# Optimization experiments

Hardware: AMD Instinct MI355X
Metric: run time of the kernel (lower is better)

The kernel has to match this reference:

```python
import jax, jax.numpy as jnp
import numpy as np

B, L, C = 512, 2048, 32  # batch, seq_len, num_labels


def setup_inputs() -> dict:
    key = jax.random.key(0)
    k1, k2, k3 = jax.random.split(key, 3)
    emissions = jax.random.normal(k1, (B, L, C), dtype=jnp.float32)
    tags = jax.random.randint(k2, (B, L), 0, C, dtype=jnp.int32)
    mask = jnp.ones((B, L), dtype=jnp.int32)
    # learned parameter: transitions (num_labels, num_labels)
    transitions = jax.random.normal(k3, (C, C), dtype=jnp.float32)
    return {"emissions": emissions, "transitions": transitions, "tags": tags, "mask": mask}


def _crf_nll(emissions, transitions, tags, mask):
    Bn, Ln, Cn = emissions.shape
    maskf = mask.astype(emissions.dtype)

    # ---- gold-path score (vectorized over the t loop) ----
    # emit[b,t] = emissions[b,t,tags[b,t]] for t in [0, L-2]
    emit = jnp.take_along_axis(emissions[:, : Ln - 1], tags[:, : Ln - 1, None], axis=2)[..., 0]
    # trans[b,t] = transitions[tags[b,t], tags[b,t+1]]
    trans = transitions[tags[:, : Ln - 1], tags[:, 1:]]
    score = jnp.sum(emit * maskf[:, : Ln - 1] + trans * maskf[:, 1:], axis=1)

    msum = jnp.sum(mask, axis=1)
    last_idx = jnp.clip(msum - 1, 0)  # index of last valid tag
    last_tag = jnp.take_along_axis(tags, last_idx[:, None], axis=1)[:, 0]
    le_t = jnp.clip(msum, 1) - 1
    last_emission = emissions[jnp.arange(Bn), le_t, last_tag]
    score = score + last_emission

    # ---- log-partition via forward algorithm (lax.scan over time) ----
    # Faithful to source: alpha_t[b,n,p] = alpha[b,p] + transitions[n,p] + emit[b,n],
    # reduced over p; the source's mask line is an algebraic no-op (a*m + a*(1-m) = a).
    def step(alpha, emit_t):
        # alpha: (B, C) over prev label p; emit_t: (B, C) over next label n
        alpha_new = jax.nn.logsumexp(alpha[:, None, :] + transitions[None, :, :], axis=2) + emit_t
        return alpha_new, None

    alpha0 = emissions[:, 0]                      # (B, C)
    em_rest = jnp.swapaxes(emissions[:, 1:], 0, 1)  # (L-1, B, C)
    alpha, _ = jax.lax.scan(step, alpha0, em_rest)
    log_Z = jax.nn.logsumexp(alpha, axis=1)       # (B,)

    return jnp.mean(log_Z - score)


def reference(emissions, transitions, tags, mask):
    return _crf_nll(emissions, transitions, tags, mask)
```

## Files before the change

kernel.cpp:

```cpp
#include <hip/hip_runtime.h>
#include <stdint.h>

typedef short bf16x8 __attribute__((ext_vector_type(8)));
typedef float f32x16 __attribute__((ext_vector_type(16)));

#define LOG2E 1.44269504088896340736f

constexpr int Bn = 512;
constexpr int Ln = 2048;
constexpr int Cn = 32;
constexpr int NSEG = 256;
constexpr int SEGLEN = 8;
constexpr int WARM = 8;
constexpr int NGRP = 16;
constexpr int DEPTH = 3;

__device__ __forceinline__ uint32_t pack2_bf16(float lo, float hi) {
    uint32_t a = __float_as_uint(lo) + 0x8000u;
    uint32_t b = __float_as_uint(hi) + 0x8000u;
    return __builtin_amdgcn_perm(b, a, 0x07060302u);
}

__global__ __launch_bounds__(64, 4) void crf_scan(
    const float* __restrict__ emis, const float* __restrict__ trans,
    float* __restrict__ dDelta)
{
    const int lane = threadIdx.x;
    const int h    = lane >> 5;
    const int bl   = lane & 31;
    const int g    = blockIdx.x & (NGRP - 1);
    const int s    = blockIdx.x >> 4;
    const int b    = g * 32 + bl;
    const size_t eb = (size_t)b * Ln * Cn;

    bf16x8 A1, A2;
    {
        float e1[8], e2[8];
        #pragma unroll
        for (int j = 0; j < 8; ++j) {
            int c1 = 4 * h + (j & 3) + 8 * (j >> 2);
            e1[j] = __expf(trans[bl * Cn + c1]);
            e2[j] = __expf(trans[bl * Cn + c1 + 16]);
        }
        union { uint32_t u[4]; bf16x8 v; } ua, ub;
        #pragma unroll
        for (int q = 0; q < 4; ++q) {
            ua.u[q] = pack2_bf16(e1[2*q], e1[2*q+1]);
            ub.u[q] = pack2_bf16(e2[2*q], e2[2*q+1]);
        }
        A1 = ua.v; A2 = ub.v;
    }

    const f32x16 zeroC = {0.f,0.f,0.f,0.f,0.f,0.f,0.f,0.f,0.f,0.f,0.f,0.f,0.f,0.f,0.f,0.f};

    f32x16 Dv;
    bf16x8 B1, B2;
    float adj = 0.f;
    float4 buf[DEPTH][4];

    const int t0 = (s == 0) ? 0 : s * SEGLEN - WARM;
    const int nsteps = (s == 0) ? SEGLEN : (WARM + SEGLEN);

    auto loadEm = [&](int t, float4 (&dst)[4]) {
        const float4* p = (const float4*)(emis + eb + (size_t)t * Cn + 4 * h);
        dst[0] = p[0]; dst[1] = p[2]; dst[2] = p[4]; dst[3] = p[6];
    };

    auto packB = [&]() {
        union { uint32_t u[4]; bf16x8 v; } p1, p2;
        #pragma unroll
        for (int q = 0; q < 4; ++q) {
            p1.u[q] = pack2_bf16(Dv[2*q],     Dv[2*q + 1]);
            p2.u[q] = pack2_bf16(Dv[8 + 2*q], Dv[8 + 2*q + 1]);
        }
        B1 = p1.v; B2 = p2.v;
    };

    auto initStep = [&](const float4 (&bu)[4]) {
        #pragma unroll
        for (int q = 0; q < 4; ++q) {
            Dv[4*q+0] = __expf(bu[q].x);
            Dv[4*q+1] = __expf(bu[q].y);
            Dv[4*q+2] = __expf(bu[q].z);
            Dv[4*q+3] = __expf(bu[q].w);
        }
        packB();
    };

    auto stepMfma = [&](const float4 (&bu)[4], float a) {
        f32x16 acc = __builtin_amdgcn_mfma_f32_32x32x16_bf16(A1, B1, zeroC, 0, 0, 0);
        acc = __builtin_amdgcn_mfma_f32_32x32x16_bf16(A2, B2, acc, 0, 0, 0);
        #pragma unroll
        for (int q = 0; q < 4; ++q) {
            float x0 = exp2f(fmaf(bu[q].x, LOG2E, a));
            float x1 = exp2f(fmaf(bu[q].y, LOG2E, a));
            float x2 = exp2f(fmaf(bu[q].z, LOG2E, a));
            float x3 = exp2f(fmaf(bu[q].w, LOG2E, a));
            Dv[4*q+0] = acc[4*q+0] * x0;
            Dv[4*q+1] = acc[4*q+1] * x1;
            Dv[4*q+2] = acc[4*q+2] * x2;
            Dv[4*q+3] = acc[4*q+3] * x3;
        }
        packB();
    };

    auto sumD = [&]() {
        float t = 0.f;
        #pragma unroll
        for (int r = 0; r < 16; ++r) t += Dv[r];
        t += __shfl_xor(t, 32, 64);
        return t;
    };

    #pragma unroll
    for (int u = 0; u < DEPTH; ++u) loadEm(t0 + u, buf[u]);

    if (s == 0) {
        initStep(buf[0]);
        loadEm(t0 + DEPTH, buf[0]);
        #pragma unroll
        for (int u = 1; u < SEGLEN; ++u) {
            stepMfma(buf[u % DEPTH], 0.f);
            if (u + DEPTH < SEGLEN) loadEm(t0 + DEPTH + u, buf[u % DEPTH]);
        }
    } else {
        initStep(buf[0]);
        loadEm(t0 + DEPTH, buf[0]);
        #pragma unroll
        for (int u = 1; u < WARM; ++u) {
            stepMfma(buf[u % DEPTH], 0.f);
            loadEm(t0 + DEPTH + u, buf[u % DEPTH]);
        }
        float S = sumD();
        adj = -__log2f(S);
        #pragma unroll
        for (int u = WARM; u < WARM + SEGLEN; ++u) {
            stepMfma(buf[u % DEPTH], (u == WARM) ? adj : 0.f);
            if (u + DEPTH < WARM + SEGLEN) loadEm(t0 + DEPTH + u, buf[u % DEPTH]);
        }
    }

    float delta = __logf(sumD());
    if (lane < 32) dDelta[s * Bn + b] = delta;
}

__global__ __launch_bounds__(256) void crf_score(
    const float* __restrict__ emis, const float* __restrict__ trans,
    const int* __restrict__ tags, const int* __restrict__ mask,
    float* __restrict__ dScoreP, int* __restrict__ dMsumP)
{
    __shared__ float Tl[Cn * Cn];
    __shared__ float sred[4];
    __shared__ int   mred[4];
    const int b   = blockIdx.x >> 2;
    const int q   = blockIdx.x & 3;
    const int tid = threadIdx.x;
    for (int i = tid; i < Cn * Cn; i += 256) Tl[i] = trans[i];
    __syncthreads();

    const size_t tB = (size_t)b * Ln;
    const size_t eB = (size_t)b * Ln * Cn;
    float sc = 0.f;
    int   ms = 0;
    #pragma unroll
    for (int k = 0; k < 2; ++k) {
        int t  = q * 512 + k * 256 + tid;
        int tg = tags[tB + t];
        int mk = mask[tB + t];
        ms += mk;
        if (t < Ln - 1) {
            int tg1 = tags[tB + t + 1];
            int mk1 = mask[tB + t + 1];
            sc += (float)mk  * emis[eB + (size_t)t * Cn + tg];
            sc += (float)mk1 * Tl[(tg << 5) + tg1];
        }
    }
    #pragma unroll
    for (int o = 32; o > 0; o >>= 1) {
        sc += __shfl_down(sc, o, 64);
        ms += __shfl_down(ms, o, 64);
    }
    if ((tid & 63) == 0) { sred[tid >> 6] = sc; mred[tid >> 6] = ms; }
    __syncthreads();
    if (tid == 0) {
        float S = 0.f; int M = 0;
        #pragma unroll
        for (int w = 0; w < 4; ++w) { S += sred[w]; M += mred[w]; }
        dScoreP[blockIdx.x] = S;
        dMsumP [blockIdx.x] = M;
    }
}

__global__ void crf_final(const float* __restrict__ dDelta,
                          const float* __restrict__ dScoreP,
                          const int* __restrict__ dMsumP,
                          const int* __restrict__ tags,
                          const float* __restrict__ emis,
                          float* __restrict__ out)
{
    __shared__ float red[8];
    int b = threadIdx.x;
    float lz = 0.f;
    #pragma unroll 8
    for (int s2 = 0; s2 < NSEG; ++s2) lz += dDelta[s2 * Bn + b];
    float sc = 0.f; int ms = 0;
    #pragma unroll
    for (int q = 0; q < 4; ++q) { sc += dScoreP[b * 4 + q]; ms += dMsumP[b * 4 + q]; }
    int last_idx = max(ms - 1, 0);
    int le_t     = max(ms, 1) - 1;
    int lt = tags[(size_t)b * Ln + last_idx];
    float le = emis[((size_t)b * Ln + le_t) * Cn + lt];
    float val = lz - (sc + le);
    #pragma unroll
    for (int o = 32; o > 0; o >>= 1) val += __shfl_down(val, o, 64);
    if ((b & 63) == 0) red[b >> 6] = val;
    __syncthreads();
    if (b == 0) {
        float t = 0.f;
        #pragma unroll
        for (int w = 0; w < 8; ++w) t += red[w];
        out[0] = t * (1.0f / (float)Bn);
    }
}

extern "C" void kernel_launch(void* const* d_in, const int* in_sizes, int n_in,
                              void* d_out, int out_size, void* d_ws, size_t ws_size,
                              hipStream_t stream)
{
    const float* emis  = (const float*)d_in[0];
    const float* trans = (const float*)d_in[1];
    const int*   tags  = (const int*)d_in[2];
    const int*   mask  = (const int*)d_in[3];
    float* wsf = (float*)d_ws;
    float* dDelta  = wsf;
    float* dScoreP = wsf + NSEG * Bn;
    int*   dMsumP  = (int*)(wsf + NSEG * Bn + 2048);
    crf_scan <<<NGRP * NSEG, 64, 0, stream>>>(emis, trans, dDelta);
    crf_score<<<4 * Bn, 256, 0, stream>>>(emis, trans, tags, mask, dScoreP, dMsumP);
    crf_final<<<1, Bn, 0, stream>>>(dDelta, dScoreP, dMsumP, tags, emis, (float*)d_out);
}
```

Baseline: 249.8 us.

## Fuse gold-path scoring into scan kernel and lengthen segments to cut warmup overhead

Removes the separate crf_score kernel. The gold-path score and mask sum are now computed inside crf_scan from emission values already loaded for the forward recurrence, using a cross-half shuffle to select the tag's emission. Segments grow from 8 to 16 steps with 128 segments, so the fixed 8-step warmup is paid over more useful steps, and the prefetch depth rises to 8. The cost is more registers per thread (occupancy hint lowered to 2), extra shuffles and LDS transition lookups inside the recurrence, and a larger per-segment reduction in crf_final.

```diff
diff --git a/kernel.cpp b/kernel.cpp
--- a/kernel.cpp
+++ b/kernel.cpp
@@ -9,11 +9,11 @@
 constexpr int Bn = 512;
 constexpr int Ln = 2048;
 constexpr int Cn = 32;
-constexpr int NSEG = 256;
-constexpr int SEGLEN = 8;
+constexpr int NSEG = 128;
+constexpr int SEGLEN = 16;
 constexpr int WARM = 8;
 constexpr int NGRP = 16;
-constexpr int DEPTH = 3;
+constexpr int DEPTH = 8;
 
 __device__ __forceinline__ uint32_t pack2_bf16(float lo, float hi) {
     uint32_t a = __float_as_uint(lo) + 0x8000u;
@@ -21,10 +21,12 @@
     return __builtin_amdgcn_perm(b, a, 0x07060302u);
 }
 
-__global__ __launch_bounds__(64, 4) void crf_scan(
+__global__ __launch_bounds__(64, 2) void crf_scan(
     const float* __restrict__ emis, const float* __restrict__ trans,
-    float* __restrict__ dDelta)
+    const int* __restrict__ tags, const int* __restrict__ mask,
+    float* __restrict__ dDelta, float* __restrict__ dScore, int* __restrict__ dMsum)
 {
+    __shared__ float Tl[Cn * Cn];
     const int lane = threadIdx.x;
     const int h    = lane >> 5;
     const int bl   = lane & 31;
@@ -32,6 +34,31 @@
     const int s    = blockIdx.x >> 4;
     const int b    = g * 32 + bl;
     const size_t eb = (size_t)b * Ln * Cn;
+    const size_t tB = (size_t)b * Ln;
+
+    for (int i = lane; i < Cn * Cn; i += 64) Tl[i] = trans[i];
+
+    const int rt0 = s * SEGLEN;
+    int tg[16], mk[16];
+    {
+        int4 a0 = *(const int4*)(tags + tB + rt0);
+        int4 a1 = *(const int4*)(tags + tB + rt0 + 4);
+        int4 a2 = *(const int4*)(tags + tB + rt0 + 8);
+        int4 a3 = *(const int4*)(tags + tB + rt0 + 12);
+        int4 c0 = *(const int4*)(mask + tB + rt0);
+        int4 c1 = *(const int4*)(mask + tB + rt0 + 4);
+        int4 c2 = *(const int4*)(mask + tB + rt0 + 8);
+        int4 c3 = *(const int4*)(mask + tB + rt0 + 12);
+        tg[0]=a0.x; tg[1]=a0.y; tg[2]=a0.z; tg[3]=a0.w;
+        tg[4]=a1.x; tg[5]=a1.y; tg[6]=a1.z; tg[7]=a1.w;
+        tg[8]=a2.x; tg[9]=a2.y; tg[10]=a2.z; tg[11]=a2.w;
+        tg[12]=a3.x; tg[13]=a3.y; tg[14]=a3.z; tg[15]=a3.w;
+        mk[0]=c0.x; mk[1]=c0.y; mk[2]=c0.z; mk[3]=c0.w;
+        mk[4]=c1.x; mk[5]=c1.y; mk[6]=c1.z; mk[7]=c1.w;
+        mk[8]=c2.x; mk[9]=c2.y; mk[10]=c2.z; mk[11]=c2.w;
+        mk[12]=c3.x; mk[13]=c3.y; mk[14]=c3.z; mk[15]=c3.w;
+    }
+    int prevTag = (s > 0) ? tags[tB + rt0 - 1] : 0;
 
     bf16x8 A1, A2;
     {
@@ -56,10 +83,11 @@
     f32x16 Dv;
     bf16x8 B1, B2;
     float adj = 0.f;
+    float sc  = 0.f;
+    int   ms  = 0;
     float4 buf[DEPTH][4];
 
-    const int t0 = (s == 0) ? 0 : s * SEGLEN - WARM;
-    const int nsteps = (s == 0) ? SEGLEN : (WARM + SEGLEN);
+    const int t0 = (s == 0) ? 0 : rt0 - WARM;
 
     auto loadEm = [&](int t, float4 (&dst)[4]) {
         const float4* p = (const float4*)(emis + eb + (size_t)t * Cn + 4 * h);
@@ -112,100 +140,93 @@
         return t;
     };
 
+    auto emitSel = [&](const float4 (&bu)[4], int tag) -> float {
+        float4 f01 = (tag & 8)  ? bu[1] : bu[0];
+        float4 f23 = (tag & 8)  ? bu[3] : bu[2];
+        float4 f   = (tag & 16) ? f23 : f01;
+        float  v0  = (tag & 1)  ? f.y : f.x;
+        float  v1  = (tag & 1)  ? f.w : f.z;
+        float  v   = (tag & 2)  ? v1 : v0;
+        float  other = __shfl_xor(v, 32, 64);
+        return (((tag >> 2) & 1) == h) ? v : other;
+    };
+
+    auto scoreStep = [&](const float4 (&bu)[4], int u) {
+        int t  = rt0 + u;
+        int tgv = tg[u], mkv = mk[u];
+        float term = 0.f;
+        if (t > 0)      term += Tl[(prevTag << 5) + tgv];
+        if (t < Ln - 1) term += emitSel(bu, tgv);
+        sc += (float)mkv * term;
+        ms += mkv;
+        prevTag = tgv;
+    };
+
     #pragma unroll
     for (int u = 0; u < DEPTH; ++u) loadEm(t0 + u, buf[u]);
 
     if (s == 0) {
+        scoreStep(buf[0], 0);
         initStep(buf[0]);
-        loadEm(t0 + DEPTH, buf[0]);
-        #pragma unroll
-        for (int u = 1; u < SEGLEN; ++u) {
-            stepMfma(buf[u % DEPTH], 0.f);
-            if (u + DEPTH < SEGLEN) loadEm(t0 + DEPTH + u, buf[u % DEPTH]);
+        loadEm(8, buf[0]);
+        #pragma unroll
+        for (int u = 1; u < 8; ++u) {
+            scoreStep(buf[u], u);
+            stepMfma(buf[u], 0.f);
+            loadEm(8 + u, buf[u]);
+        }
+        #pragma unroll
+        for (int u = 8; u < 16; ++u) {
+            scoreStep(buf[u & 7], u);
+            stepMfma(buf[u & 7], 0.f);
         }
     } else {
         initStep(buf[0]);
-        loadEm(t0 + DEPTH, buf[0]);
+        loadEm(t0 + 8, buf[0]);
         #pragma unroll
         for (int u = 1; u < WARM; ++u) {
-            stepMfma(buf[u % DEPTH], 0.f);
-            loadEm(t0 + DEPTH + u, buf[u % DEPTH]);
+            stepMfma(buf[u], 0.f);
+            loadEm(t0 + 8 + u, buf[u]);
         }
         float S = sumD();
         adj = -__log2f(S);
         #pragma unroll
-        for (int u = WARM; u < WARM + SEGLEN; ++u) {
-            stepMfma(buf[u % DEPTH], (u == WARM) ? adj : 0.f);
-            if (u + DEPTH < WARM + SEGLEN) loadEm(t0 + DEPTH + u, buf[u % DEPTH]);
+        for (int u = 0; u < 8; ++u) {
+            scoreStep(buf[u], u);
+            stepMfma(buf[u], (u == 0) ? adj : 0.f);
+            loadEm(rt0 + 8 + u, buf[u]);
+        }
+        #pragma unroll
+        for (int u = 8; u < 16; ++u) {
+            scoreStep(buf[u & 7], u);
+            stepMfma(buf[u & 7], 0.f);
         }
     }
 
     float delta = __logf(sumD());
-    if (lane < 32) dDelta[s * Bn + b] = delta;
-}
-
-__global__ __launch_bounds__(256) void crf_score(
-    const float* __restrict__ emis, const float* __restrict__ trans,
-    const int* __restrict__ tags, const int* __restrict__ mask,
-    float* __restrict__ dScoreP, int* __restrict__ dMsumP)
-{
-    __shared__ float Tl[Cn * Cn];
-    __shared__ float sred[4];
-    __shared__ int   mred[4];
-    const int b   = blockIdx.x >> 2;
-    const int q   = blockIdx.x & 3;
-    const int tid = threadIdx.x;
-    for (int i = tid; i < Cn * Cn; i += 256) Tl[i] = trans[i];
-    __syncthreads();
-
-    const size_t tB = (size_t)b * Ln;
-    const size_t eB = (size_t)b * Ln * Cn;
-    float sc = 0.f;
-    int   ms = 0;
-    #pragma unroll
-    for (int k = 0; k < 2; ++k) {
-        int t  = q * 512 + k * 256 + tid;
-        int tg = tags[tB + t];
-        int mk = mask[tB + t];
-        ms += mk;
-        if (t < Ln - 1) {
-            int tg1 = tags[tB + t + 1];
-            int mk1 = mask[tB + t + 1];
-            sc += (float)mk  * emis[eB + (size_t)t * Cn + tg];
-            sc += (float)mk1 * Tl[(tg << 5) + tg1];
-        }
-    }
-    #pragma unroll
-    for (int o = 32; o > 0; o >>= 1) {
-        sc += __shfl_down(sc, o, 64);
-        ms += __shfl_down(ms, o, 64);
-    }
-    if ((tid & 63) == 0) { sred[tid >> 6] = sc; mred[tid >> 6] = ms; }
-    __syncthreads();
-    if (tid == 0) {
-        float S = 0.f; int M = 0;
-        #pragma unroll
-        for (int w = 0; w < 4; ++w) { S += sred[w]; M += mred[w]; }
-        dScoreP[blockIdx.x] = S;
-        dMsumP [blockIdx.x] = M;
+    if (lane < 32) {
+        dDelta[s * Bn + b] = delta;
+        dScore[s * Bn + b] = sc;
+        dMsum [s * Bn + b] = ms;
     }
 }
 
 __global__ void crf_final(const float* __restrict__ dDelta,
-                          const float* __restrict__ dScoreP,
-                          const int* __restrict__ dMsumP,
+                          const float* __restrict__ dScore,
+                          const int* __restrict__ dMsum,
                           const int* __restrict__ tags,
                           const float* __restrict__ emis,
                           float* __restrict__ out)
 {
     __shared__ float red[8];
     int b = threadIdx.x;
-    float lz = 0.f;
+    float lz = 0.f, sc = 0.f; int ms = 0;
     #pragma unroll 8
-    for (int s2 = 0; s2 < NSEG; ++s2) lz += dDelta[s2 * Bn + b];
-    float sc = 0.f; int ms = 0;
-    #pragma unroll
-    for (int q = 0; q < 4; ++q) { sc += dScoreP[b * 4 + q]; ms += dMsumP[b * 4 + q]; }
+    for (int s2 = 0; s2 < NSEG; ++s2) {
+        lz += dDelta[s2 * Bn + b];
+        sc += dScore[s2 * Bn + b];
+        ms += dMsum [s2 * Bn + b];
+    }
     int last_idx = max(ms - 1, 0);
     int le_t     = max(ms, 1) - 1;
     int lt = tags[(size_t)b * Ln + last_idx];
@@ -232,10 +253,9 @@
     const int*   tags  = (const int*)d_in[2];
     const int*   mask  = (const int*)d_in[3];
     float* wsf = (float*)d_ws;
-    float* dDelta  = wsf;
-    float* dScoreP = wsf + NSEG * Bn;
-    int*   dMsumP  = (int*)(wsf + NSEG * Bn + 2048);
-    crf_scan <<<NGRP * NSEG, 64, 0, stream>>>(emis, trans, dDelta);
-    crf_score<<<4 * Bn, 256, 0, stream>>>(emis, trans, tags, mask, dScoreP, dMsumP);
-    crf_final<<<1, Bn, 0, stream>>>(dDelta, dScoreP, dMsumP, tags, emis, (float*)d_out);
-}
+    float* dDelta = wsf;
+    float* dScore = wsf + NSEG * Bn;
+    int*   dMsum  = (int*)(wsf + 2 * NSEG * Bn);
+    crf_scan <<<NGRP * NSEG, 64, 0, stream>>>(emis, trans, tags, mask, dDelta, dScore, dMsum);
+    crf_final<<<1, Bn, 0, stream>>>(dDelta, dScore, dMsum, tags, emis, (float*)d_out);
+}
```

New measurement: 284.2 us. +13.7%, slower.
